# Kernel optimization log

Hardware: AMD Instinct MI355X
Metric: run time of the kernel (lower is better)

## Reference

```python
import jax, jax.numpy as jnp
import numpy as np

N_NODES = 100000
N_EDGES = 1600000
IN_FEATS = 128
OUT_FEATS = 128


def setup_inputs() -> dict:
    key = jax.random.key(0)
    k1, k2, k3, k4, k5 = jax.random.split(key, 5)
    feat = jax.random.normal(k1, (N_NODES, IN_FEATS), dtype=jnp.float32)
    # He (kaiming) uniform-ish init scale for the weights
    bound = np.sqrt(6.0 / IN_FEATS).astype(np.float32)
    weight_u = jax.random.uniform(k2, (IN_FEATS, OUT_FEATS), jnp.float32, -bound, bound)
    weight_v = jax.random.uniform(k3, (IN_FEATS, OUT_FEATS), jnp.float32, -bound, bound)
    bias = jnp.zeros((OUT_FEATS,), dtype=jnp.float32)
    src = jax.random.randint(k4, (N_EDGES,), 0, N_NODES, dtype=jnp.int32)
    dst = jax.random.randint(k5, (N_EDGES,), 0, N_NODES, dtype=jnp.int32)
    return {"feat": feat, "weight_u": weight_u, "weight_v": weight_v,
            "bias": bias, "src": src, "dst": dst}


def reference(feat, weight_u, weight_v, bias, src, dst):
    n = feat.shape[0]
    # in_feats (128) is not > out_feats (128) -> aggregate first, then matmul
    # m_i = sum_{j in N(i)} h_j  (copy_u + sum over edges)
    agg = jax.ops.segment_sum(feat[src], dst, num_segments=n)  # [N, in_feats]
    rst_u = jnp.matmul(agg, weight_u)                          # [N, out_feats]
    rst_v = jnp.matmul(feat, weight_v)                         # [N, out_feats]
    # in-degree normalization, clamped at 1
    deg = jax.ops.segment_sum(jnp.ones_like(dst, dtype=feat.dtype), dst,
                              num_segments=n)
    norm = 1.0 / jnp.maximum(deg, 1.0)                         # [N]
    out = jax.nn.relu(rst_v + norm[:, None] * rst_u + bias)
    return out
```

## Files before the change

kernel.cpp:

```cpp
#include <hip/hip_runtime.h>
#include <hip/hip_bf16.h>
#include <stdint.h>

#define NN 100000
#define NE 1600000
#define NF 128
#define NTILE ((NN + 63) / 64)
#define GEMM_G 782
#define B_BKT 1563
#define NB2 128
#define EPB (NE / NB2)
#define NCNT (B_BKT * NB2)
#define SC2A ((NCNT + 255) / 256)
#define CONV4 (NN * NF / 4)
#define CONV_BLK ((CONV4 + 255) / 256)
#define SETUP_GRID (NB2 + 16 + CONV_BLK)
#define CAP 3072

typedef __attribute__((ext_vector_type(8))) __bf16 bf16x8;
typedef __attribute__((ext_vector_type(4))) float floatx4;
typedef __attribute__((ext_vector_type(4))) unsigned short ushortx4;
typedef __attribute__((ext_vector_type(8))) unsigned short ushortx8;

static __device__ __forceinline__ unsigned short f2bf(float x) {
    union { float f; unsigned u; } v; v.f = x;
    unsigned r = v.u + 0x7fffu + ((v.u >> 16) & 1u);
    return (unsigned short)(r >> 16);
}
static __device__ __forceinline__ float bflo(unsigned w) {
    union { unsigned u; float f; } v; v.u = w << 16; return v.f;
}
static __device__ __forceinline__ float bfhi(unsigned w) {
    union { unsigned u; float f; } v; v.u = w & 0xffff0000u; return v.f;
}

__global__ void k_setup(const float* __restrict__ feat, unsigned short* __restrict__ featb,
                        const float* __restrict__ wv, const float* __restrict__ wu,
                        unsigned short* __restrict__ w2t,
                        const int* __restrict__ dst, int* __restrict__ counts) {
    __shared__ int h[B_BKT];
    int b = blockIdx.x;
    int tid = threadIdx.x;
    if (b < NB2) {
        for (int i = tid; i < B_BKT; i += 256) h[i] = 0;
        __syncthreads();
        int base = b * EPB, end = base + EPB;
        for (int i = base + tid; i < end; i += 256) {
            int d = __builtin_nontemporal_load(&dst[i]);
            atomicAdd(&h[d >> 6], 1);
        }
        __syncthreads();
        for (int i = tid; i < B_BKT; i += 256)
            counts[i * NB2 + b] = h[i];
    } else if (b < NB2 + 16) {
        int id = (b - NB2) * 256 + tid;
        if (id < 128 * 32) {
            int n = id >> 5, kg = id & 31;
            const float* srcm = (kg < 16) ? wv : wu;
            int k0 = (kg & 15) * 8;
            ushortx8 o;
#pragma unroll
            for (int j = 0; j < 8; ++j)
                o[j] = f2bf(srcm[(k0 + j) * 128 + n]);
            int dchunk = n * 32 + (kg ^ (n & 7));
            *(ushortx8*)(w2t + dchunk * 8) = o;
        }
    } else {
        int i = (b - NB2 - 16) * 256 + tid;
        if (i < CONV4) {
            floatx4 f = __builtin_nontemporal_load((const floatx4*)feat + i);
            ushortx4 o;
            o.x = f2bf(f.x); o.y = f2bf(f.y); o.z = f2bf(f.z); o.w = f2bf(f.w);
            __builtin_nontemporal_store(o, (ushortx4*)featb + i);
        }
    }
}

__global__ void k_scan2_a(int* __restrict__ counts, int* __restrict__ bsums) {
    __shared__ int sh[256];
    int i = blockIdx.x * 256 + threadIdx.x;
    int v = (i < NCNT) ? counts[i] : 0;
    sh[threadIdx.x] = v;
    __syncthreads();
    for (int off = 1; off < 256; off <<= 1) {
        int u = (threadIdx.x >= off) ? sh[threadIdx.x - off] : 0;
        __syncthreads();
        sh[threadIdx.x] += u;
        __syncthreads();
    }
    if (i < NCNT) counts[i] = sh[threadIdx.x] - v;
    if (threadIdx.x == 255) bsums[blockIdx.x] = sh[255];
}
__global__ void k_scan2_b(int* __restrict__ bsums) {
    __shared__ int sh[1024];
    int t = threadIdx.x;
    int v = (t < SC2A) ? bsums[t] : 0;
    sh[t] = v;
    __syncthreads();
    for (int off = 1; off < 1024; off <<= 1) {
        int u = (t >= off) ? sh[t - off] : 0;
        __syncthreads();
        sh[t] += u;
        __syncthreads();
    }
    if (t < SC2A) bsums[t] = sh[t] - v;
}

__global__ void k_binscatter(const int* __restrict__ src, const int* __restrict__ dst,
                             const int* __restrict__ counts, const int* __restrict__ bsums,
                             unsigned* __restrict__ streams) {
    __shared__ int cur[B_BKT];
    int tid = threadIdx.x;
    for (int i = tid; i < B_BKT; i += 512) {
        int idx = i * NB2 + blockIdx.x;
        cur[i] = counts[idx] + bsums[idx >> 8];
    }
    __syncthreads();
    int base = blockIdx.x * EPB, end = base + EPB;
    for (int i = base + tid; i < end; i += 512) {
        int d = __builtin_nontemporal_load(&dst[i]);
        int s = __builtin_nontemporal_load(&src[i]);
        int b = d >> 6;
        unsigned packed = ((unsigned)(d & 63) << 17) | (unsigned)s;
        int pos = atomicAdd(&cur[b], 1);
        streams[pos] = packed;
    }
}

__global__ void k_aggsort(const unsigned* __restrict__ streams,
                          const int* __restrict__ counts, const int* __restrict__ bsums,
                          const unsigned short* __restrict__ featb,
                          unsigned short* __restrict__ aggb) {
    __shared__ int hist[64];
    __shared__ int nodeoff[65];
    __shared__ int eb[CAP];
    __shared__ int nextn;
    int tid = threadIdx.x;
    int bkt = blockIdx.x;
    int idx = bkt * NB2;
    int s = counts[idx] + bsums[idx >> 8];
    int e = (bkt == B_BKT - 1) ? NE : (counts[idx + NB2] + bsums[(idx + NB2) >> 8]);
    int seg = e - s;
    int lane = tid & 63, wave = tid >> 6;

    if (tid < 64) hist[tid] = 0;
    if (tid == 0) nextn = 0;
    __syncthreads();
    for (int i = s + tid; i < e; i += 256)
        atomicAdd(&hist[streams[i] >> 17], 1);
    __syncthreads();
    if (tid == 0) {
        int run = 0;
#pragma unroll
        for (int n = 0; n < 64; ++n) { nodeoff[n] = run; run += hist[n]; }
        nodeoff[64] = run;
    }
    __syncthreads();
    if (tid < 64) hist[tid] = nodeoff[tid];
    __syncthreads();

    if (seg <= CAP) {
        for (int i = s + tid; i < e; i += 256) {
            unsigned v = streams[i];
            int p = atomicAdd(&hist[v >> 17], 1);
            eb[p] = (int)(v & 0x1FFFFu);
        }
        __syncthreads();
        for (;;) {
            int nl;
            if (lane == 0) nl = atomicAdd(&nextn, 1);
            nl = __shfl(nl, 0, 64);
            if (nl >= 64) break;
            int node = bkt * 64 + nl;
            if (node >= NN) continue;
            int s0 = nodeoff[nl], s1 = nodeoff[nl + 1];
            float a0 = 0.f, a1 = 0.f;
            for (int base = s0; base < s1; base += 64) {
                int ee = (base + lane < s1) ? eb[base + lane] : 0;
                int m = s1 - base; if (m > 64) m = 64;
                int j = 0;
                for (; j + 8 <= m; j += 8) {
                    unsigned w0 = *(const unsigned*)(featb + (size_t)__shfl(ee, j + 0, 64) * NF + lane * 2);
                    unsigned w1 = *(const unsigned*)(featb + (size_t)__shfl(ee, j + 1, 64) * NF + lane * 2);
                    unsigned w2 = *(const unsigned*)(featb + (size_t)__shfl(ee, j + 2, 64) * NF + lane * 2);
                    unsigned w3 = *(const unsigned*)(featb + (size_t)__shfl(ee, j + 3, 64) * NF + lane * 2);
                    unsigned w4 = *(const unsigned*)(featb + (size_t)__shfl(ee, j + 4, 64) * NF + lane * 2);
                    unsigned w5 = *(const unsigned*)(featb + (size_t)__shfl(ee, j + 5, 64) * NF + lane * 2);
                    unsigned w6 = *(const unsigned*)(featb + (size_t)__shfl(ee, j + 6, 64) * NF + lane * 2);
                    unsigned w7 = *(const unsigned*)(featb + (size_t)__shfl(ee, j + 7, 64) * NF + lane * 2);
                    a0 += bflo(w0) + bflo(w1) + bflo(w2) + bflo(w3)
                        + bflo(w4) + bflo(w5) + bflo(w6) + bflo(w7);
                    a1 += bfhi(w0) + bfhi(w1) + bfhi(w2) + bfhi(w3)
                        + bfhi(w4) + bfhi(w5) + bfhi(w6) + bfhi(w7);
                }
                for (; j < m; ++j) {
                    int nn = __shfl(ee, j, 64);
                    unsigned w = *(const unsigned*)(featb + (size_t)nn * NF + lane * 2);
                    a0 += bflo(w); a1 += bfhi(w);
                }
            }
            int dg = s1 - s0; if (dg < 1) dg = 1;
            float scale = 1.0f / (float)dg;
            unsigned outw = ((unsigned)f2bf(a1 * scale) << 16) | (unsigned)f2bf(a0 * scale);
            *(unsigned*)(aggb + (size_t)node * NF + lane * 2) = outw;
        }
    } else {
        for (int nl = wave * 16; nl < wave * 16 + 16; ++nl) {
            int node = bkt * 64 + nl;
            if (node >= NN) break;
            float a0 = 0.f, a1 = 0.f;
            int dg = 0;
            for (int i = s; i < e; ++i) {
                unsigned v = streams[i];
                if ((int)(v >> 17) == nl) {
                    ++dg;
                    unsigned w = *(const unsigned*)(featb + (size_t)(v & 0x1FFFFu) * NF + lane * 2);
                    a0 += bflo(w); a1 += bfhi(w);
                }
            }
            int dc = dg < 1 ? 1 : dg;
            float scale = 1.0f / (float)dc;
            unsigned outw = ((unsigned)f2bf(a1 * scale) << 16) | (unsigned)f2bf(a0 * scale);
            *(unsigned*)(aggb + (size_t)node * NF + lane * 2) = outw;
        }
    }
}

static __device__ __forceinline__ void gemm_tile(
    const unsigned short* lds, const bf16x8* a, const float* bsv,
    int rb, int quad, int l15, float* __restrict__ out) {
    floatx4 acc[8];
#pragma unroll
    for (int ct = 0; ct < 8; ++ct) acc[ct] = (floatx4){0.f, 0.f, 0.f, 0.f};
#pragma unroll
    for (int ct = 0; ct < 8; ++ct) {
        int n = ct * 16 + l15;
        int rowoff = n << 8;
        int sw = n & 7;
#pragma unroll
        for (int ks = 0; ks < 8; ++ks) {
            int kg = ks * 4 + quad;
            bf16x8 b = *(const bf16x8*)(&lds[rowoff + ((kg ^ sw) << 3)]);
            acc[ct] = __builtin_amdgcn_mfma_f32_16x16x32_bf16(a[ks], b, acc[ct], 0, 0, 0);
        }
    }
#pragma unroll
    for (int r = 0; r < 4; ++r) {
        int row = rb + quad * 4 + r;
        if (row < NN) {
#pragma unroll
            for (int ct = 0; ct < 8; ++ct) {
                int col = ct * 16 + l15;
                float v = acc[ct][r] + bsv[ct];
                out[(size_t)row * NF + col] = v > 0.f ? v : 0.f;
            }
        }
    }
}

__global__ __launch_bounds__(256, 2) void k_gemm(
    const unsigned short* __restrict__ featb,
    const unsigned short* __restrict__ aggb,
    const unsigned short* __restrict__ w2t,
    const float* __restrict__ bias,
    float* __restrict__ out) {
    __shared__ unsigned short lds[128 * 256];
    for (int i = threadIdx.x; i < 4096; i += 256) {
        ushortx8 w = *(const ushortx8*)(w2t + i * 8);
        *(ushortx8*)(&lds[i * 8]) = w;
    }
    __syncthreads();

    int lane = threadIdx.x & 63;
    int wave = threadIdx.x >> 6;
    int quad = lane >> 4, l15 = lane & 15;

    float bsv[8];
#pragma unroll
    for (int ct = 0; ct < 8; ++ct) bsv[ct] = bias[ct * 16 + l15];

    int t0 = blockIdx.x;
    int t1 = t0 + GEMM_G;
    int t1v = (t1 < NTILE) ? t1 : t0;

    int rb0 = t0 * 64 + wave * 16;
    int rb1 = t1v * 64 + wave * 16;
    int ar0 = rb0 + l15; if (ar0 > NN - 1) ar0 = NN - 1;
    int ar1 = rb1 + l15; if (ar1 > NN - 1) ar1 = NN - 1;
    const unsigned short* fr0 = featb + (size_t)ar0 * NF;
    const unsigned short* ag0 = aggb + (size_t)ar0 * NF;
    const unsigned short* fr1 = featb + (size_t)ar1 * NF;
    const unsigned short* ag1 = aggb + (size_t)ar1 * NF;

    bf16x8 a0[8], a1[8];
#pragma unroll
    for (int ks = 0; ks < 4; ++ks) {
        a0[ks]     = *(const bf16x8*)(fr0 + ks * 32 + quad * 8);
        a0[4 + ks] = *(const bf16x8*)(ag0 + ks * 32 + quad * 8);
    }
#pragma unroll
    for (int ks = 0; ks < 4; ++ks) {
        a1[ks]     = *(const bf16x8*)(fr1 + ks * 32 + quad * 8);
        a1[4 + ks] = *(const bf16x8*)(ag1 + ks * 32 + quad * 8);
    }

    gemm_tile(lds, a0, bsv, rb0, quad, l15, out);
    if (t1 < NTILE)
        gemm_tile(lds, a1, bsv, rb1, quad, l15, out);
}

extern "C" void kernel_launch(void* const* d_in, const int* in_sizes, int n_in,
                              void* d_out, int out_size, void* d_ws, size_t ws_size,
                              hipStream_t stream) {
    const float* feat = (const float*)d_in[0];
    const float* wu   = (const float*)d_in[1];
    const float* wv   = (const float*)d_in[2];
    const float* bias = (const float*)d_in[3];
    const int* src    = (const int*)d_in[4];
    const int* dst    = (const int*)d_in[5];
    float* out        = (float*)d_out;

    char* ws = (char*)d_ws;
    int* counts           = (int*)(ws + 0);
    int* bsums            = (int*)(ws + 800256);
    unsigned* streams     = (unsigned*)(ws + 1204480);
    unsigned short* featb = (unsigned short*)(ws + 7604480);
    unsigned short* aggb  = (unsigned short*)(ws + 33204480);
    unsigned short* w2t   = (unsigned short*)(ws + 58804480);

    k_setup<<<SETUP_GRID, 256, 0, stream>>>(feat, featb, wv, wu, w2t, dst, counts);
    k_scan2_a<<<SC2A, 256, 0, stream>>>(counts, bsums);
    k_scan2_b<<<1, 1024, 0, stream>>>(bsums);
    k_binscatter<<<NB2, 512, 0, stream>>>(src, dst, counts, bsums, streams);
    k_aggsort<<<B_BKT, 256, 0, stream>>>(streams, counts, bsums, featb, aggb);
    k_gemm<<<GEMM_G, 256, 0, stream>>>(featb, aggb, w2t, bias, out);
}
```

Before: 287.7 us.

## Fuse aggregation and GEMM into one kernel with LDS-resident agg tile

```diff
diff --git a/kernel.cpp b/kernel.cpp
--- a/kernel.cpp
+++ b/kernel.cpp
@@ -5,8 +5,6 @@
 #define NN 100000
 #define NE 1600000
 #define NF 128
-#define NTILE ((NN + 63) / 64)
-#define GEMM_G 782
 #define B_BKT 1563
 #define NB2 128
 #define EPB (NE / NB2)
@@ -127,13 +125,17 @@
     }
 }
 
-__global__ void k_aggsort(const unsigned* __restrict__ streams,
-                          const int* __restrict__ counts, const int* __restrict__ bsums,
-                          const unsigned short* __restrict__ featb,
-                          unsigned short* __restrict__ aggb) {
+__global__ __launch_bounds__(256, 4) void k_agggemm(
+    const unsigned* __restrict__ streams,
+    const int* __restrict__ counts, const int* __restrict__ bsums,
+    const unsigned short* __restrict__ featb,
+    const unsigned short* __restrict__ w2t,
+    const float* __restrict__ bias,
+    float* __restrict__ out) {
     __shared__ int hist[64];
     __shared__ int nodeoff[65];
     __shared__ int eb[CAP];
+    __shared__ unsigned short aggt[64 * NF];
     __shared__ int nextn;
     int tid = threadIdx.x;
     int bkt = blockIdx.x;
@@ -202,7 +204,7 @@
             int dg = s1 - s0; if (dg < 1) dg = 1;
             float scale = 1.0f / (float)dg;
             unsigned outw = ((unsigned)f2bf(a1 * scale) << 16) | (unsigned)f2bf(a0 * scale);
-            *(unsigned*)(aggb + (size_t)node * NF + lane * 2) = outw;
+            *(unsigned*)((char*)aggt + nl * 256 + ((lane * 4) ^ ((nl & 7) << 4))) = outw;
         }
     } else {
         for (int nl = wave * 16; nl < wave * 16 + 16; ++nl) {
@@ -221,92 +223,50 @@
             int dc = dg < 1 ? 1 : dg;
             float scale = 1.0f / (float)dc;
             unsigned outw = ((unsigned)f2bf(a1 * scale) << 16) | (unsigned)f2bf(a0 * scale);
-            *(unsigned*)(aggb + (size_t)node * NF + lane * 2) = outw;
-        }
-    }
-}
-
-static __device__ __forceinline__ void gemm_tile(
-    const unsigned short* lds, const bf16x8* a, const float* bsv,
-    int rb, int quad, int l15, float* __restrict__ out) {
-    floatx4 acc[8];
-#pragma unroll
-    for (int ct = 0; ct < 8; ++ct) acc[ct] = (floatx4){0.f, 0.f, 0.f, 0.f};
-#pragma unroll
+            *(unsigned*)((char*)aggt + nl * 256 + ((lane * 4) ^ ((nl & 7) << 4))) = outw;
+        }
+    }
+    __syncthreads();
+
+    int quad = lane >> 4, l15 = lane & 15;
+    int rbl = wave * 16;
+    int rb = bkt * 64 + rbl;
+    int ar = rb + l15; if (ar > NN - 1) ar = NN - 1;
+    const unsigned short* fr = featb + (size_t)ar * NF;
+    int lrow = rbl + l15;
+    bf16x8 a[8];
+#pragma unroll
+    for (int ks = 0; ks < 4; ++ks)
+        a[ks] = *(const bf16x8*)(fr + ks * 32 + quad * 8);
+#pragma unroll
+    for (int ks = 0; ks < 4; ++ks) {
+        int boff = (ks * 64 + quad * 16) ^ ((lrow & 7) << 4);
+        a[4 + ks] = *(const bf16x8*)((const char*)aggt + lrow * 256 + boff);
+    }
+    float bsv[8];
+#pragma unroll
+    for (int ct = 0; ct < 8; ++ct) bsv[ct] = bias[ct * 16 + l15];
+#pragma unroll 1
     for (int ct = 0; ct < 8; ++ct) {
         int n = ct * 16 + l15;
-        int rowoff = n << 8;
+        const unsigned short* wrow = w2t + (n << 8);
         int sw = n & 7;
+        floatx4 acc = (floatx4){0.f, 0.f, 0.f, 0.f};
 #pragma unroll
         for (int ks = 0; ks < 8; ++ks) {
             int kg = ks * 4 + quad;
-            bf16x8 b = *(const bf16x8*)(&lds[rowoff + ((kg ^ sw) << 3)]);
-            acc[ct] = __builtin_amdgcn_mfma_f32_16x16x32_bf16(a[ks], b, acc[ct], 0, 0, 0);
-        }
-    }
-#pragma unroll
-    for (int r = 0; r < 4; ++r) {
-        int row = rb + quad * 4 + r;
-        if (row < NN) {
-#pragma unroll
-            for (int ct = 0; ct < 8; ++ct) {
-                int col = ct * 16 + l15;
-                float v = acc[ct][r] + bsv[ct];
-                out[(size_t)row * NF + col] = v > 0.f ? v : 0.f;
+            bf16x8 b = *(const bf16x8*)(wrow + ((kg ^ sw) << 3));
+            acc = __builtin_amdgcn_mfma_f32_16x16x32_bf16(a[ks], b, acc, 0, 0, 0);
+        }
+#pragma unroll
+        for (int r = 0; r < 4; ++r) {
+            int row = rb + quad * 4 + r;
+            if (row < NN) {
+                float v = acc[r] + bsv[ct];
+                out[(size_t)row * NF + ct * 16 + l15] = v > 0.f ? v : 0.f;
             }
         }
     }
-}
-
-__global__ __launch_bounds__(256, 2) void k_gemm(
-    const unsigned short* __restrict__ featb,
-    const unsigned short* __restrict__ aggb,
-    const unsigned short* __restrict__ w2t,
-    const float* __restrict__ bias,
-    float* __restrict__ out) {
-    __shared__ unsigned short lds[128 * 256];
-    for (int i = threadIdx.x; i < 4096; i += 256) {
-        ushortx8 w = *(const ushortx8*)(w2t + i * 8);
-        *(ushortx8*)(&lds[i * 8]) = w;
-    }
-    __syncthreads();
-
-    int lane = threadIdx.x & 63;
-    int wave = threadIdx.x >> 6;
-    int quad = lane >> 4, l15 = lane & 15;
-
-    float bsv[8];
-#pragma unroll
-    for (int ct = 0; ct < 8; ++ct) bsv[ct] = bias[ct * 16 + l15];
-
-    int t0 = blockIdx.x;
-    int t1 = t0 + GEMM_G;
-    int t1v = (t1 < NTILE) ? t1 : t0;
-
-    int rb0 = t0 * 64 + wave * 16;
-    int rb1 = t1v * 64 + wave * 16;
-    int ar0 = rb0 + l15; if (ar0 > NN - 1) ar0 = NN - 1;
-    int ar1 = rb1 + l15; if (ar1 > NN - 1) ar1 = NN - 1;
-    const unsigned short* fr0 = featb + (size_t)ar0 * NF;
-    const unsigned short* ag0 = aggb + (size_t)ar0 * NF;
-    const unsigned short* fr1 = featb + (size_t)ar1 * NF;
-    const unsigned short* ag1 = aggb + (size_t)ar1 * NF;
-
-    bf16x8 a0[8], a1[8];
-#pragma unroll
-    for (int ks = 0; ks < 4; ++ks) {
-        a0[ks]     = *(const bf16x8*)(fr0 + ks * 32 + quad * 8);
-        a0[4 + ks] = *(const bf16x8*)(ag0 + ks * 32 + quad * 8);
-    }
-#pragma unroll
-    for (int ks = 0; ks < 4; ++ks) {
-        a1[ks]     = *(const bf16x8*)(fr1 + ks * 32 + quad * 8);
-        a1[4 + ks] = *(const bf16x8*)(ag1 + ks * 32 + quad * 8);
-    }
-
-    gemm_tile(lds, a0, bsv, rb0, quad, l15, out);
-    if (t1 < NTILE)
-        gemm_tile(lds, a1, bsv, rb1, quad, l15, out);
 }
 
 extern "C" void kernel_launch(void* const* d_in, const int* in_sizes, int n_in,
@@ -325,13 +285,11 @@
     int* bsums            = (int*)(ws + 800256);
     unsigned* streams     = (unsigned*)(ws + 1204480);
     unsigned short* featb = (unsigned short*)(ws + 7604480);
-    unsigned short* aggb  = (unsigned short*)(ws + 33204480);
     unsigned short* w2t   = (unsigned short*)(ws + 58804480);
 
     k_setup<<<SETUP_GRID, 256, 0, stream>>>(feat, featb, wv, wu, w2t, dst, counts);
     k_scan2_a<<<SC2A, 256, 0, stream>>>(counts, bsums);
     k_scan2_b<<<1, 1024, 0, stream>>>(bsums);
     k_binscatter<<<NB2, 512, 0, stream>>>(src, dst, counts, bsums, streams);
-    k_aggsort<<<B_BKT, 256, 0, stream>>>(streams, counts, bsums, featb, aggb);
-    k_gemm<<<GEMM_G, 256, 0, stream>>>(featb, aggb, w2t, bias, out);
-}
+    k_agggemm<<<B_BKT, 256, 0, stream>>>(streams, counts, bsums, featb, w2t, bias, out);
+}
```

New measurement: 289.2 us. About the same (+0.5%).
